# Kernel optimization log

Hardware: AMD Instinct MI355X
Metric: run time of the kernel (lower is better)

The kernel has to match this reference:

```python
import jax, jax.numpy as jnp
import numpy as np

PATCH = 3  # patch_size=3, stride=1
B, C, H, W = 8, 256, 64, 64


def _extract_patches(x):
    # x: (c, h, w) -> (c*PATCH*PATCH, N) with N = (h-2)*(w-2), valid 3x3 patches
    c, h, w = x.shape
    hh, ww = h - PATCH + 1, w - PATCH + 1
    pats = jnp.stack([x[:, i:i + hh, j:j + ww]
                      for i in range(PATCH) for j in range(PATCH)], axis=0)  # (9, c, hh, ww)
    return pats.reshape(PATCH * PATCH * c, hh * ww)


def _index_to_flow(max_idx):
    # max_idx: (hh, ww) int -> flow (h, w, 2) padded by 2 at bottom/right
    hh, ww = max_idx.shape
    flow_w = (max_idx % ww).astype(jnp.float32)
    flow_h = (max_idx // ww).astype(jnp.float32)
    gy, gx = jnp.meshgrid(jnp.arange(hh, dtype=jnp.float32),
                          jnp.arange(ww, dtype=jnp.float32), indexing='ij')
    flow = jnp.stack((flow_w - gx, flow_h - gy), axis=2)  # (hh, ww, 2)
    return jnp.pad(flow, ((0, 2), (0, 2), (0, 0)))


def _per_image(feat_in, feat_ref):
    c, h, w = feat_in.shape
    hh, ww = h - PATCH + 1, w - PATCH + 1
    # channel-wise L2 normalize each spatial position (F.normalize dim=0, eps=1e-12)
    feat_in = feat_in / jnp.maximum(jnp.linalg.norm(feat_in, axis=0, keepdims=True), 1e-12)
    feat_ref = feat_ref / jnp.maximum(jnp.linalg.norm(feat_ref, axis=0, keepdims=True), 1e-12)
    Pi = _extract_patches(feat_in)    # (k, N)
    Pr = _extract_patches(feat_ref)   # (k, N)
    # is_norm=True: normalize ref patches (norm + 1e-5, per BasicSR feature_match_index)
    Pr = Pr / (jnp.linalg.norm(Pr, axis=0, keepdims=True) + 1e-5)
    corr = Pi.T @ Pr                  # (N, N) exhaustive patch correlation
    max_val = corr.max(axis=1)
    max_idx = jnp.argmax(corr, axis=1)
    # norm_input=True: divide by input patch norms
    max_val = max_val / jnp.linalg.norm(Pi, axis=0)
    max_val = max_val.reshape(hh, ww)
    max_idx = max_idx.reshape(hh, ww)
    sim = jnp.pad(max_val, ((1, 1), (1, 1)))[None]  # (1, h, w)
    flow = _index_to_flow(max_idx)                   # (h, w, 2)
    # nine down-right shifts (fill 0 at top-left), tensor_shift semantics
    shifted = jnp.stack([jnp.pad(flow[:h - i, :w - j], ((i, 0), (j, 0), (0, 0)))
                         for i in range(3) for j in range(3)], axis=0)  # (9, h, w, 2)
    return flow, shifted, sim


def setup_inputs() -> dict:
    key = jax.random.key(0)
    k1, k2 = jax.random.split(key)
    features1 = jax.random.normal(k1, (B, C, H, W), dtype=jnp.float32)
    features2 = jax.random.normal(k2, (B, C, H, W), dtype=jnp.float32)
    return {"features1": features1, "features2": features2}


def reference(features1, features2):
    pre_flow, pre_offset, pre_similarity = jax.vmap(_per_image)(features1, features2)
    # pre_flow: (b,h,w,2); pre_offset: (b,9,h,w,2); pre_similarity: (b,1,h,w)
    return pre_flow, pre_offset, pre_similarity
```

## Files before the change

kernel.cpp:

```cpp
#include <hip/hip_runtime.h>

typedef unsigned short u16;
typedef unsigned char u8;
typedef unsigned int u32;
typedef __bf16 bf16x8 __attribute__((ext_vector_type(8)));
typedef float f32x4 __attribute__((ext_vector_type(4)));

constexpr int BATCH = 8;
constexpr int C = 256;
constexpr int H = 64;
constexpr int W = 64;
constexpr int HW = H * W;
constexpr int HH = 62, WW = 62;
constexpr int NQ = HH * WW;
constexpr int SEG = 8;
constexpr int NBLK_RED = 536;

constexpr size_t OFF_RNORM = 0;
constexpr size_t OFF_RESV = 262144;
constexpr size_t OFF_RESI = 385280;
constexpr size_t OFF_SLOT0 = 508416;
constexpr size_t SP_H1 = 0;
constexpr size_t SP_L1 = 2097152;
constexpr size_t SP_H2 = 4194304;
constexpr size_t SP_L2 = 6291456;
constexpr size_t SP_P = 8388608;
constexpr size_t SP_PIDX8 = 75497472;
constexpr size_t SLOT_BYTES = 77594624;

typedef const __attribute__((address_space(1))) unsigned int* gas_ptr;
typedef __attribute__((address_space(3))) unsigned int* las_ptr;
__device__ __forceinline__ void gl16(const void* g, void* l) {
  __builtin_amdgcn_global_load_lds((gas_ptr)g, (las_ptr)l, 16, 0, 0);
}

__device__ __forceinline__ int pre_of(int ki) {
  if (ki <= 62) return ki * (ki + 1) / 2;
  int r = 123 - ki;
  return 1953 + 1891 - r * (r + 1) / 2;
}

__global__ __launch_bounds__(256) void norm_kernel(const float* __restrict__ f1,
                                                   const float* __restrict__ f2,
                                                   float* __restrict__ rnorm) {
  int by = blockIdx.x;
  int tensor = blockIdx.y;
  const float* f = tensor ? f2 : f1;
  int b = by >> 6, y = by & 63;
  int x = threadIdx.x & 63;
  int cq = threadIdx.x >> 6;
  const float* base = f + ((size_t)b * C) * HW + y * W + x;
  float s = 0.f;
  for (int c = cq; c < C; c += 4) {
    float v = base[(size_t)c * HW];
    s = fmaf(v, v, s);
  }
  __shared__ float sm[4][64];
  sm[cq][x] = s;
  __syncthreads();
  if (threadIdx.x < 64) {
    float t = sm[0][x] + sm[1][x] + sm[2][x] + sm[3][x];
    float nrm = fmaxf(sqrtf(t), 1e-12f);
    rnorm[((size_t)tensor * BATCH + b) * HW + y * W + x] = 1.0f / nrm;
  }
}

__global__ __launch_bounds__(256) void convert_kernel(const float* __restrict__ f1,
                                                      const float* __restrict__ f2,
                                                      const float* __restrict__ rnorm,
                                                      int b0, char* __restrict__ slot0) {
  int chunk = blockIdx.x;
  int tensor = blockIdx.y;
  int sloti = blockIdx.z;
  int bi = b0 + sloti;
  char* slot = slot0 + (size_t)sloti * SLOT_BYTES;
  int pos0 = chunk * 32;
  const float* f = (tensor ? f2 : f1) + (size_t)bi * C * HW;
  const float* rn = rnorm + ((size_t)tensor * BATCH + bi) * HW + pos0;
  u16* dh = (u16*)(slot + (tensor ? SP_H2 : SP_H1)) + (size_t)pos0 * C;
  u16* dl = (u16*)(slot + (tensor ? SP_L2 : SP_L1)) + (size_t)pos0 * C;

  __shared__ u32 sm[32][257];
  int t = threadIdx.x;
  int px = t & 31, cg = t >> 5;
  float r = rn[px];
  for (int kk = 0; kk < 32; ++kk) {
    int c = (cg << 5) + kk;
    float v = f[(size_t)c * HW + pos0 + px] * r;
    __bf16 h = (__bf16)v;
    float hf = (float)h;
    __bf16 lo = (__bf16)(v - hf);
    sm[px][c] = ((u32)__builtin_bit_cast(u16, h) << 16) | (u32)__builtin_bit_cast(u16, lo);
  }
  __syncthreads();
  int px2 = t >> 3, seg = t & 7;
  int c0 = seg * 32;
  for (int g8 = 0; g8 < 4; ++g8) {
    u32 hw0, hw1, hw2, hw3, lw0, lw1, lw2, lw3;
    u32 a, b2;
    a = sm[px2][c0 + g8 * 8 + 0]; b2 = sm[px2][c0 + g8 * 8 + 1];
    hw0 = (a >> 16) | (b2 & 0xFFFF0000u); lw0 = (a & 0xFFFFu) | (b2 << 16);
    a = sm[px2][c0 + g8 * 8 + 2]; b2 = sm[px2][c0 + g8 * 8 + 3];
    hw1 = (a >> 16) | (b2 & 0xFFFF0000u); lw1 = (a & 0xFFFFu) | (b2 << 16);
    a = sm[px2][c0 + g8 * 8 + 4]; b2 = sm[px2][c0 + g8 * 8 + 5];
    hw2 = (a >> 16) | (b2 & 0xFFFF0000u); lw2 = (a & 0xFFFFu) | (b2 << 16);
    a = sm[px2][c0 + g8 * 8 + 6]; b2 = sm[px2][c0 + g8 * 8 + 7];
    hw3 = (a >> 16) | (b2 & 0xFFFF0000u); lw3 = (a & 0xFFFFu) | (b2 << 16);
    size_t off = (size_t)px2 * C + c0 + g8 * 8;
    uint4 hv; hv.x = hw0; hv.y = hw1; hv.z = hw2; hv.w = hw3;
    uint4 lv; lv.x = lw0; lv.y = lw1; lv.z = lw2; lv.w = lw3;
    *(uint4*)(dh + off) = hv;
    *(uint4*)(dl + off) = lv;
  }
}

__global__ __launch_bounds__(256, 2) void pgemm_kernel(char* __restrict__ slot0) {
  char* slot = slot0 + (size_t)blockIdx.y * SLOT_BYTES;
  const u16* hi1 = (const u16*)(slot + SP_H1);
  const u16* lo1 = (const u16*)(slot + SP_L1);
  const u16* hi2 = (const u16*)(slot + SP_H2);
  const u16* lo2 = (const u16*)(slot + SP_L2);
  float* P = (float*)(slot + SP_P);

  int bid = blockIdx.x;
  int swz = (bid & 7) * 128 + (bid >> 3);
  int p0 = (swz >> 5) << 7, q0 = (swz & 31) << 7;

  __shared__ __align__(16) char smem[65536];

  int t = threadIdx.x;
  int l = t & 63, w = t >> 6, wm = w >> 1, wn = w & 1;
  int lr = l & 15, lh = l >> 4;

  const u16* srcs[4] = {hi1 + (size_t)p0 * 256, lo1 + (size_t)p0 * 256,
                        hi2 + (size_t)q0 * 256, lo2 + (size_t)q0 * 256};

  f32x4 acc[4][4];
#pragma unroll
  for (int mf = 0; mf < 4; ++mf)
#pragma unroll
    for (int nf = 0; nf < 4; ++nf)
      acc[mf][nf] = (f32x4){0.f, 0.f, 0.f, 0.f};

  auto stage = [&](int b, int kt) {
    char* base = smem + b * 32768;
#pragma unroll
    for (int pl = 0; pl < 4; ++pl) {
      const u16* s = srcs[pl];
#pragma unroll
      for (int wq = 0; wq < 2; ++wq) {
        int ci = (w * 2 + wq) * 64 + l;
        int row = ci >> 2, sl = ci & 3;
        int q = sl ^ ((row >> 1) & 3);
        size_t goff = (size_t)row * 256 + kt * 32 + (q << 3);
        gl16(s + goff, base + pl * 8192 + (w * 2 + wq) * 1024 + l * 16);
      }
    }
  };

  stage(0, 0);
  __syncthreads();

  for (int kt = 0; kt < 8; ++kt) {
    int b = kt & 1;
    if (kt < 7) stage(b ^ 1, kt + 1);
    char* sAh = smem + b * 32768;
    char* sAl = sAh + 8192;
    char* sBh = sAh + 16384;
    char* sBl = sAh + 24576;
    bf16x8 ah[4], al[4];
#pragma unroll
    for (int mf = 0; mf < 4; ++mf) {
      int row = wm * 64 + mf * 16 + lr;
      int off = row * 64 + ((lh ^ ((row >> 1) & 3)) << 4);
      ah[mf] = *(const bf16x8*)(sAh + off);
      al[mf] = *(const bf16x8*)(sAl + off);
    }
#pragma unroll
    for (int nf = 0; nf < 4; ++nf) {
      int row = wn * 64 + nf * 16 + lr;
      int off = row * 64 + ((lh ^ ((row >> 1) & 3)) << 4);
      bf16x8 bh = *(const bf16x8*)(sBh + off);
      bf16x8 bl = *(const bf16x8*)(sBl + off);
#pragma unroll
      for (int mf = 0; mf < 4; ++mf) {
        acc[mf][nf] = __builtin_amdgcn_mfma_f32_16x16x32_bf16(ah[mf], bh, acc[mf][nf], 0, 0, 0);
        acc[mf][nf] = __builtin_amdgcn_mfma_f32_16x16x32_bf16(al[mf], bh, acc[mf][nf], 0, 0, 0);
        acc[mf][nf] = __builtin_amdgcn_mfma_f32_16x16x32_bf16(ah[mf], bl, acc[mf][nf], 0, 0, 0);
      }
    }
    __syncthreads();
  }

  float* sq = (float*)smem;
#pragma unroll
  for (int pass = 0; pass < 2; ++pass) {
    if (pass) __syncthreads();
    if (wn == pass) {
      float* buf = sq + wm * 4352;
#pragma unroll
      for (int mf = 0; mf < 4; ++mf)
#pragma unroll
        for (int nf = 0; nf < 4; ++nf)
#pragma unroll
          for (int j = 0; j < 4; ++j)
            buf[(mf * 16 + lh * 4 + j) * 68 + nf * 16 + lr] = acc[mf][nf][j];
      *(f32x4*)(buf + l * 68 + 64) = (f32x4){0.f, 0.f, 0.f, 0.f};
    }
    __syncthreads();
    int tid2 = t & 127, sel = t >> 7;
    int ax = tid2 & 63, halfj = tid2 >> 6;
    const float* S = sq + sel * 4352;
    int rr1 = ax + 1 > 63 ? 63 : ax + 1;
    int rr2 = ax + 2 > 63 ? 63 : ax + 2;
    const float* S0 = S + ax * 68;
    const float* S1 = S + rr1 * 68;
    const float* S2 = S + rr2 * 68;
    int planeIdx = (((p0 >> 6) + sel) << 6) + (q0 >> 6) + pass;
    float* Qp = P + (((size_t)planeIdx) << 12);
#pragma unroll
    for (int gi = 0; gi < 4; ++gi) {
      int g = halfj * 4 + gi;
      int c0 = g * 8;
      float r0[12], r1a[12], r2a[12];
#pragma unroll
      for (int u = 0; u < 3; ++u) {
        *(f32x4*)(r0 + u * 4) = *(const f32x4*)(S0 + c0 + u * 4);
        *(f32x4*)(r1a + u * 4) = *(const f32x4*)(S1 + c0 + u * 4);
        *(f32x4*)(r2a + u * 4) = *(const f32x4*)(S2 + c0 + u * 4);
      }
      f32x4 qv0, qv1;
#pragma unroll
      for (int e = 0; e < 4; ++e) qv0[e] = r0[e] + r1a[e + 1] + r2a[e + 2];
#pragma unroll
      for (int e = 0; e < 4; ++e) qv1[e] = r0[e + 4] + r1a[e + 5] + r2a[e + 6];
      float* Qg = Qp + g * 512 + (ax << 2);
      __builtin_nontemporal_store(qv0, (f32x4*)(Qg));
      __builtin_nontemporal_store(qv1, (f32x4*)(Qg + 256));
    }
  }
}

__global__ __launch_bounds__(512) void reduce_kernel(char* __restrict__ slot0,
                                                     size_t slotBytes) {
  int slot = blockIdx.y;
  char* sb = slot0 + (size_t)slot * slotBytes;
  const float* QT = (const float*)(sb + SP_P);
  float* pval8 = (float*)sb;
  u8* pidx8 = (u8*)(sb + SP_PIDX8);

  int bid = blockIdx.x;
  int ki = 0;
  for (ki = 0; ki < 123; ++ki) {
    int d = ki - 61; if (d < 0) d = -d;
    int ns = (62 - d + SEG - 1) / SEG;
    if (bid < ns) break;
    bid -= ns;
  }
  int k = ki - 61;
  int ystart = k < 0 ? -k : 0;
  int yend = k > 0 ? 61 - k : 61;
  int y0 = ystart + bid * SEG;
  int y1 = y0 + SEG; if (y1 > yend + 1) y1 = yend + 1;
  int sid0 = pre_of(ki) + (y0 - ystart);
  int pmax = yend + 2;

  int t = threadIdx.x;
  int w = t >> 6, l = t & 63;

  float A[8], B[8], P0[8], P1[8], P2[8];

  auto ld = [&](int p, float* D) {
    const float* gp = QT + (((size_t)((p << 6) + (p + k))) << 12) + (w << 9) + (l << 2);
    *(f32x4*)(D) = __builtin_nontemporal_load((const f32x4*)gp);
    *(f32x4*)(D + 4) = __builtin_nontemporal_load((const f32x4*)(gp + 256));
  };

  auto candstep = [&](int y, const float* D0, const float* D1, const float* D2) {
    float best = __uint_as_float(0xFF800000u);
    int bbb = 0;
#pragma unroll
    for (int s = 0; s < 8; ++s) {
      float c = D0[s] + D1[s] + D2[s];
      bool valid = (w * 8 + s) <= 61;
      if (valid && c > best) { best = c; bbb = s; }
    }
    size_t o = (size_t)(sid0 + (y - y0)) * 512 + (w << 6) + l;
    pval8[o] = best;
    pidx8[o] = (u8)bbb;
  };

  ld(y0, A);
  ld(y0 + 1, B);
  ld(y0 + 2, P0);
  ld(y0 + 3 > pmax ? pmax : y0 + 3, P1);
  ld(y0 + 4 > pmax ? pmax : y0 + 4, P2);

  int y = y0;
  while (true) {
    candstep(y, A, B, P0);
#pragma unroll
    for (int s = 0; s < 8; ++s) { A[s] = B[s]; B[s] = P0[s]; }
    if (++y >= y1) break;
    ld(y + 4 > pmax ? pmax : y + 4, P0);
    candstep(y, A, B, P1);
#pragma unroll
    for (int s = 0; s < 8; ++s) { A[s] = B[s]; B[s] = P1[s]; }
    if (++y >= y1) break;
    ld(y + 4 > pmax ? pmax : y + 4, P1);
    candstep(y, A, B, P2);
#pragma unroll
    for (int s = 0; s < 8; ++s) { A[s] = B[s]; B[s] = P2[s]; }
    if (++y >= y1) break;
    ld(y + 4 > pmax ? pmax : y + 4, P2);
  }
}

__global__ __launch_bounds__(256) void combine_kernel(const char* __restrict__ slot0,
                                                      size_t slotBytes, int b0,
                                                      float* __restrict__ resv,
                                                      int* __restrict__ residx) {
  int q = blockIdx.x * 256 + threadIdx.x;
  if (q >= NQ) return;
  int slot = blockIdx.y;
  int b = b0 + slot;
  const char* sb = slot0 + (size_t)slot * slotBytes;
  const float* pval8 = (const float*)sb;
  const u8* pidx8 = (const u8*)(sb + SP_PIDX8);
  int y = q / 62, ax = q - y * 62;
  float best = __uint_as_float(0xFF800000u);
  int bjy = 0, bw = 0;
  for (int jy = 0; jy < 62; ++jy) {
    int ki = 61 + jy - y;
    int sid = pre_of(ki) + (y < jy ? y : jy);
    const float* p = pval8 + (size_t)sid * 512 + ax;
#pragma unroll
    for (int ww = 0; ww < 8; ++ww) {
      float v = p[ww << 6];
      if (v > best) { best = v; bjy = jy; bw = ww; }
    }
  }
  int kib = 61 + bjy - y;
  int sidb = pre_of(kib) + (y < bjy ? y : bjy);
  int bb = pidx8[(size_t)sidb * 512 + (bw << 6) + ax];
  resv[(size_t)b * NQ + q] = best;
  residx[(size_t)b * NQ + q] = bjy * 62 + bw * 8 + bb;
}

__global__ __launch_bounds__(256) void assemble_kernel(const float* __restrict__ res_val,
                                                       const int* __restrict__ res_idx,
                                                       float* __restrict__ out) {
  int gid = blockIdx.x * 256 + threadIdx.x;
  if (gid >= BATCH * HW) return;
  int b = gid >> 12;
  int y = (gid >> 6) & 63;
  int x = gid & 63;

  float* out_flow = out;
  float* out_off = out + (size_t)BATCH * HW * 2;
  float* out_sim = out + (size_t)BATCH * HW * 2 + (size_t)BATCH * 9 * HW * 2;

  auto flow_at = [&](int yy, int xx, float* fx, float* fy) {
    if (yy >= 0 && yy < HH && xx >= 0 && xx < WW) {
      int idx = res_idx[(size_t)b * NQ + yy * WW + xx];
      *fx = (float)(idx % WW - xx);
      *fy = (float)(idx / WW - yy);
    } else {
      *fx = 0.f;
      *fy = 0.f;
    }
  };

  float fx, fy;
  flow_at(y, x, &fx, &fy);
  size_t fo = ((size_t)b * HW + y * W + x) * 2;
  out_flow[fo + 0] = fx;
  out_flow[fo + 1] = fy;

#pragma unroll
  for (int sft = 0; sft < 9; ++sft) {
    int i = sft / 3, j = sft % 3;
    float ox, oy;
    flow_at(y - i, x - j, &ox, &oy);
    size_t o = (((size_t)b * 9 + sft) * HW + y * W + x) * 2;
    out_off[o + 0] = ox;
    out_off[o + 1] = oy;
  }

  float sim = 0.f;
  if (y >= 1 && y <= HH && x >= 1 && x <= WW) {
    float mv = res_val[(size_t)b * NQ + (y - 1) * WW + (x - 1)];
    sim = mv * (1.0f / ((3.0f + 1e-5f) * 3.0f));
  }
  out_sim[(size_t)b * HW + y * W + x] = sim;
}

extern "C" void kernel_launch(void* const* d_in, const int* in_sizes, int n_in,
                              void* d_out, int out_size, void* d_ws, size_t ws_size,
                              hipStream_t stream) {
  const float* f1 = (const float*)d_in[0];
  const float* f2 = (const float*)d_in[1];
  float* out = (float*)d_out;
  char* ws = (char*)d_ws;

  float* rnorm = (float*)(ws + OFF_RNORM);
  float* resv = (float*)(ws + OFF_RESV);
  int* residx = (int*)(ws + OFF_RESI);
  char* slot0 = ws + OFF_SLOT0;

  int nslots = 1;
  if (ws_size > OFF_SLOT0 + SLOT_BYTES) {
    size_t n = (ws_size - OFF_SLOT0) / SLOT_BYTES;
    nslots = n >= 8 ? 8 : (int)n;
    if (nslots < 1) nslots = 1;
  }

  norm_kernel<<<dim3(BATCH * H, 2), 256, 0, stream>>>(f1, f2, rnorm);

  for (int b0 = 0; b0 < BATCH; b0 += nslots) {
    int g = BATCH - b0 < nslots ? BATCH - b0 : nslots;
    convert_kernel<<<dim3(128, 2, g), 256, 0, stream>>>(f1, f2, rnorm, b0, slot0);
    pgemm_kernel<<<dim3(1024, g), 256, 0, stream>>>(slot0);
    reduce_kernel<<<dim3(NBLK_RED, g), 512, 0, stream>>>(slot0, SLOT_BYTES);
    combine_kernel<<<dim3(16, g), 256, 0, stream>>>(slot0, SLOT_BYTES, b0,
                                                    resv, residx);
  }

  int total = BATCH * HW;
  assemble_kernel<<<(total + 255) / 256, 256, 0, stream>>>(resv, residx, out);
}
```

Measured before the change: 544.1 us.

## Software-pipeline convert, GEMM and reduce across images in one merged kernel

Replaces the per-batch sequence of convert, pgemm and reduce launches with a single merged kernel per step. Each launch runs the GEMM for image i, the reduction for image i-1 and the conversion for image i+1, using two double-buffered slots and a separate per-image partial-result buffer for the combine step. The reduce body now has each 256-thread block cover 16 columns per lane (two warp groups) instead of using 512 threads. The aim is to overlap the memory-bound reduce with the compute-bound GEMM and to remove the large multi-slot workspace. In exchange, each stage of the pipeline adds a launch, and mixing block roles in one grid gives every block the GEMM's shared memory and register budget, which may lower occupancy for the reduce and convert blocks.

```diff
diff --git a/kernel.cpp b/kernel.cpp
--- a/kernel.cpp
+++ b/kernel.cpp
@@ -19,14 +19,17 @@
 constexpr size_t OFF_RNORM = 0;
 constexpr size_t OFF_RESV = 262144;
 constexpr size_t OFF_RESI = 385280;
-constexpr size_t OFF_SLOT0 = 508416;
+constexpr size_t OFF_PV = 508416;
+constexpr size_t OFF_PI = OFF_PV + 62980096;
+constexpr size_t OFF_SLOT0 = OFF_PI + 15745024;
 constexpr size_t SP_H1 = 0;
 constexpr size_t SP_L1 = 2097152;
 constexpr size_t SP_H2 = 4194304;
 constexpr size_t SP_L2 = 6291456;
-constexpr size_t SP_P = 8388608;
-constexpr size_t SP_PIDX8 = 75497472;
-constexpr size_t SLOT_BYTES = 77594624;
+constexpr size_t SP_Q = 8388608;
+constexpr size_t SLOT_BYTES = 75513856;
+
+constexpr size_t PVIMG = (size_t)NQ * 512;
 
 typedef const __attribute__((address_space(1))) unsigned int* gas_ptr;
 typedef __attribute__((address_space(3))) unsigned int* las_ptr;
@@ -65,23 +68,19 @@
   }
 }
 
-__global__ __launch_bounds__(256) void convert_kernel(const float* __restrict__ f1,
-                                                      const float* __restrict__ f2,
-                                                      const float* __restrict__ rnorm,
-                                                      int b0, char* __restrict__ slot0) {
-  int chunk = blockIdx.x;
-  int tensor = blockIdx.y;
-  int sloti = blockIdx.z;
-  int bi = b0 + sloti;
-  char* slot = slot0 + (size_t)sloti * SLOT_BYTES;
+__device__ __forceinline__ void convert_body(int chunk, int tensor, int bi,
+                                             const float* __restrict__ f1,
+                                             const float* __restrict__ f2,
+                                             const float* __restrict__ rnorm,
+                                             char* slot, char* smemraw, int t) {
+  typedef u32 row_t[257];
+  row_t* sm = (row_t*)smemraw;
   int pos0 = chunk * 32;
   const float* f = (tensor ? f2 : f1) + (size_t)bi * C * HW;
   const float* rn = rnorm + ((size_t)tensor * BATCH + bi) * HW + pos0;
   u16* dh = (u16*)(slot + (tensor ? SP_H2 : SP_H1)) + (size_t)pos0 * C;
   u16* dl = (u16*)(slot + (tensor ? SP_L2 : SP_L1)) + (size_t)pos0 * C;
 
-  __shared__ u32 sm[32][257];
-  int t = threadIdx.x;
   int px = t & 31, cg = t >> 5;
   float r = rn[px];
   for (int kk = 0; kk < 32; ++kk) {
@@ -114,21 +113,16 @@
   }
 }
 
-__global__ __launch_bounds__(256, 2) void pgemm_kernel(char* __restrict__ slot0) {
-  char* slot = slot0 + (size_t)blockIdx.y * SLOT_BYTES;
+__device__ __forceinline__ void pgemm_body(int bid, char* slot, char* smem, int t) {
   const u16* hi1 = (const u16*)(slot + SP_H1);
   const u16* lo1 = (const u16*)(slot + SP_L1);
   const u16* hi2 = (const u16*)(slot + SP_H2);
   const u16* lo2 = (const u16*)(slot + SP_L2);
-  float* P = (float*)(slot + SP_P);
-
-  int bid = blockIdx.x;
+  float* P = (float*)(slot + SP_Q);
+
   int swz = (bid & 7) * 128 + (bid >> 3);
   int p0 = (swz >> 5) << 7, q0 = (swz & 31) << 7;
 
-  __shared__ __align__(16) char smem[65536];
-
-  int t = threadIdx.x;
   int l = t & 63, w = t >> 6, wm = w >> 1, wn = w & 1;
   int lr = l & 15, lh = l >> 4;
 
@@ -241,15 +235,11 @@
   }
 }
 
-__global__ __launch_bounds__(512) void reduce_kernel(char* __restrict__ slot0,
-                                                     size_t slotBytes) {
-  int slot = blockIdx.y;
-  char* sb = slot0 + (size_t)slot * slotBytes;
-  const float* QT = (const float*)(sb + SP_P);
-  float* pval8 = (float*)sb;
-  u8* pidx8 = (u8*)(sb + SP_PIDX8);
-
-  int bid = blockIdx.x;
+__device__ __forceinline__ void reduce_body(int rid, const char* slot,
+                                            float* pval8, u8* pidx8, int t) {
+  const float* QT = (const float*)(slot + SP_Q);
+
+  int bid = rid;
   int ki = 0;
   for (ki = 0; ki < 123; ++ki) {
     int d = ki - 61; if (d < 0) d = -d;
@@ -265,29 +255,36 @@
   int sid0 = pre_of(ki) + (y0 - ystart);
   int pmax = yend + 2;
 
-  int t = threadIdx.x;
-  int w = t >> 6, l = t & 63;
-
-  float A[8], B[8], P0[8], P1[8], P2[8];
+  int w2 = t >> 6, l = t & 63;
+
+  float A[16], B[16], P0[16], P1[16], P2[16];
 
   auto ld = [&](int p, float* D) {
-    const float* gp = QT + (((size_t)((p << 6) + (p + k))) << 12) + (w << 9) + (l << 2);
-    *(f32x4*)(D) = __builtin_nontemporal_load((const f32x4*)gp);
-    *(f32x4*)(D + 4) = __builtin_nontemporal_load((const f32x4*)(gp + 256));
+    const float* gp = QT + (((size_t)((p << 6) + (p + k))) << 12) + (l << 2);
+#pragma unroll
+    for (int h = 0; h < 2; ++h) {
+      const float* g2 = gp + ((w2 + h * 4) << 9);
+      *(f32x4*)(D + h * 8) = __builtin_nontemporal_load((const f32x4*)g2);
+      *(f32x4*)(D + h * 8 + 4) = __builtin_nontemporal_load((const f32x4*)(g2 + 256));
+    }
   };
 
   auto candstep = [&](int y, const float* D0, const float* D1, const float* D2) {
-    float best = __uint_as_float(0xFF800000u);
-    int bbb = 0;
-#pragma unroll
-    for (int s = 0; s < 8; ++s) {
-      float c = D0[s] + D1[s] + D2[s];
-      bool valid = (w * 8 + s) <= 61;
-      if (valid && c > best) { best = c; bbb = s; }
-    }
-    size_t o = (size_t)(sid0 + (y - y0)) * 512 + (w << 6) + l;
-    pval8[o] = best;
-    pidx8[o] = (u8)bbb;
+#pragma unroll
+    for (int h = 0; h < 2; ++h) {
+      int ww = w2 + h * 4;
+      float best = __uint_as_float(0xFF800000u);
+      int bbb = 0;
+#pragma unroll
+      for (int s = 0; s < 8; ++s) {
+        float c = D0[h * 8 + s] + D1[h * 8 + s] + D2[h * 8 + s];
+        bool valid = (ww * 8 + s) <= 61;
+        if (valid && c > best) { best = c; bbb = s; }
+      }
+      size_t o = (size_t)(sid0 + (y - y0)) * 512 + (ww << 6) + l;
+      pval8[o] = best;
+      pidx8[o] = (u8)bbb;
+    }
   };
 
   ld(y0, A);
@@ -300,33 +297,69 @@
   while (true) {
     candstep(y, A, B, P0);
 #pragma unroll
-    for (int s = 0; s < 8; ++s) { A[s] = B[s]; B[s] = P0[s]; }
+    for (int s = 0; s < 16; ++s) { A[s] = B[s]; B[s] = P0[s]; }
     if (++y >= y1) break;
     ld(y + 4 > pmax ? pmax : y + 4, P0);
     candstep(y, A, B, P1);
 #pragma unroll
-    for (int s = 0; s < 8; ++s) { A[s] = B[s]; B[s] = P1[s]; }
+    for (int s = 0; s < 16; ++s) { A[s] = B[s]; B[s] = P1[s]; }
     if (++y >= y1) break;
     ld(y + 4 > pmax ? pmax : y + 4, P1);
     candstep(y, A, B, P2);
 #pragma unroll
-    for (int s = 0; s < 8; ++s) { A[s] = B[s]; B[s] = P2[s]; }
+    for (int s = 0; s < 16; ++s) { A[s] = B[s]; B[s] = P2[s]; }
     if (++y >= y1) break;
     ld(y + 4 > pmax ? pmax : y + 4, P2);
   }
 }
 
-__global__ __launch_bounds__(256) void combine_kernel(const char* __restrict__ slot0,
-                                                      size_t slotBytes, int b0,
+__global__ __launch_bounds__(256) void convert_kernel(const float* __restrict__ f1,
+                                                      const float* __restrict__ f2,
+                                                      const float* __restrict__ rnorm,
+                                                      int bi, char* __restrict__ slot) {
+  __shared__ __align__(16) char smem[33024];
+  convert_body(blockIdx.x, blockIdx.y, bi, f1, f2, rnorm, slot, smem, threadIdx.x);
+}
+
+__global__ __launch_bounds__(256, 2) void merged_kernel(const float* __restrict__ f1,
+                                                        const float* __restrict__ f2,
+                                                        const float* __restrict__ rnorm,
+                                                        char* __restrict__ ws,
+                                                        int pg_img, int rd_img, int cv_img) {
+  __shared__ __align__(16) char smem[65536];
+  int bx = blockIdx.x, t = threadIdx.x;
+  char* slot0 = ws + OFF_SLOT0;
+
+  if (bx < 1608) {
+    int m = bx % 3;
+    if (m < 2) {
+      int pid = (bx / 3) * 2 + m;
+      if (pg_img >= 0 && pid < 1024)
+        pgemm_body(pid, slot0 + (size_t)(pg_img & 1) * SLOT_BYTES, smem, t);
+    } else {
+      int rid = bx / 3;
+      if (rd_img >= 0) {
+        float* pv = (float*)(ws + OFF_PV) + (size_t)rd_img * PVIMG;
+        u8* pi = (u8*)(ws + OFF_PI) + (size_t)rd_img * PVIMG;
+        reduce_body(rid, slot0 + (size_t)(rd_img & 1) * SLOT_BYTES, pv, pi, t);
+      }
+    }
+  } else {
+    int cid = bx - 1608;
+    if (cv_img >= 0)
+      convert_body(cid & 127, cid >> 7, cv_img, f1, f2, rnorm,
+                   slot0 + (size_t)(cv_img & 1) * SLOT_BYTES, smem, t);
+  }
+}
+
+__global__ __launch_bounds__(256) void combine_kernel(const char* __restrict__ ws,
                                                       float* __restrict__ resv,
                                                       int* __restrict__ residx) {
   int q = blockIdx.x * 256 + threadIdx.x;
   if (q >= NQ) return;
-  int slot = blockIdx.y;
-  int b = b0 + slot;
-  const char* sb = slot0 + (size_t)slot * slotBytes;
-  const float* pval8 = (const float*)sb;
-  const u8* pidx8 = (const u8*)(sb + SP_PIDX8);
+  int b = blockIdx.y;
+  const float* pval8 = (const float*)(ws + OFF_PV) + (size_t)b * PVIMG;
+  const u8* pidx8 = (const u8*)(ws + OFF_PI) + (size_t)b * PVIMG;
   int y = q / 62, ax = q - y * 62;
   float best = __uint_as_float(0xFF800000u);
   int bjy = 0, bw = 0;
@@ -379,9 +412,9 @@
 
 #pragma unroll
   for (int sft = 0; sft < 9; ++sft) {
-    int i = sft / 3, j = sft % 3;
+    int i = sft / 3, jj = sft % 3;
     float ox, oy;
-    flow_at(y - i, x - j, &ox, &oy);
+    flow_at(y - i, x - jj, &ox, &oy);
     size_t o = (((size_t)b * 9 + sft) * HW + y * W + x) * 2;
     out_off[o + 0] = ox;
     out_off[o + 1] = oy;
@@ -408,23 +441,16 @@
   int* residx = (int*)(ws + OFF_RESI);
   char* slot0 = ws + OFF_SLOT0;
 
-  int nslots = 1;
-  if (ws_size > OFF_SLOT0 + SLOT_BYTES) {
-    size_t n = (ws_size - OFF_SLOT0) / SLOT_BYTES;
-    nslots = n >= 8 ? 8 : (int)n;
-    if (nslots < 1) nslots = 1;
-  }
-
   norm_kernel<<<dim3(BATCH * H, 2), 256, 0, stream>>>(f1, f2, rnorm);
-
-  for (int b0 = 0; b0 < BATCH; b0 += nslots) {
-    int g = BATCH - b0 < nslots ? BATCH - b0 : nslots;
-    convert_kernel<<<dim3(128, 2, g), 256, 0, stream>>>(f1, f2, rnorm, b0, slot0);
-    pgemm_kernel<<<dim3(1024, g), 256, 0, stream>>>(slot0);
-    reduce_kernel<<<dim3(NBLK_RED, g), 512, 0, stream>>>(slot0, SLOT_BYTES);
-    combine_kernel<<<dim3(16, g), 256, 0, stream>>>(slot0, SLOT_BYTES, b0,
-                                                    resv, residx);
-  }
+  convert_kernel<<<dim3(128, 2), 256, 0, stream>>>(f1, f2, rnorm, 0, slot0);
+
+  for (int i = 0; i < 8; ++i) {
+    int cv = (i + 1 < 8) ? i + 1 : -1;
+    merged_kernel<<<1864, 256, 0, stream>>>(f1, f2, rnorm, ws, i, i - 1, cv);
+  }
+  merged_kernel<<<1864, 256, 0, stream>>>(f1, f2, rnorm, ws, -1, 7, -1);
+
+  combine_kernel<<<dim3(16, BATCH), 256, 0, stream>>>(ws, resv, residx);
 
   int total = BATCH * HW;
   assemble_kernel<<<(total + 255) / 256, 256, 0, stream>>>(resv, residx, out);
```

Measured after the change: 478.7 us. 12.0% less time.
